# Kernel optimization log

Measured on AMD Instinct MI355X. Metric: run time of the kernel, lower is better.

Reference implementation:

```python
import jax, jax.numpy as jnp
import numpy as np

B, N, DIM = 2, 1024, 512
HEADS, DIM_HEAD = 8, 64
HIDDEN = HEADS * DIM_HEAD
TIME_DIM = 512
BIAS_DIM = 16
EPS = 1e-5


def setup_inputs() -> dict:
    key = jax.random.key(0)
    ks = jax.random.split(key, 12)
    inp = {
        "x": jax.random.normal(ks[0], (B, N, DIM), jnp.float32),
        "residx": jnp.broadcast_to(jnp.arange(N, dtype=jnp.float32), (B, N)),
        "time": jax.random.normal(ks[1], (B, 1, TIME_DIM), jnp.float32),
        "attn_bias": jax.random.normal(ks[2], (B, BIAS_DIM, N, N), jnp.float32),
        "seq_mask": jnp.ones((B, N), jnp.float32),
        # params
        "gamma": jnp.ones((DIM,), jnp.float32),
        "Wt": jax.random.normal(ks[3], (2 * DIM, TIME_DIM), jnp.float32) * 0.02,
        "bt": jax.random.normal(ks[4], (2 * DIM,), jnp.float32) * 0.02,
        "Wb": jax.random.normal(ks[5], (HEADS, BIAS_DIM), jnp.float32) * 0.1,
        "bb": jax.random.normal(ks[6], (HEADS,), jnp.float32) * 0.1,
        "Wq": jax.random.normal(ks[7], (HIDDEN, DIM), jnp.float32) * (DIM ** -0.5),
        "Wkv": jax.random.normal(ks[8], (2 * HIDDEN, DIM), jnp.float32) * (DIM ** -0.5),
        "Wo": jax.random.normal(ks[9], (DIM, HIDDEN), jnp.float32) * (HIDDEN ** -0.5),
    }
    return inp


def _layer_norm(x, gamma):
    mu = jnp.mean(x, axis=-1, keepdims=True)
    var = jnp.var(x, axis=-1, keepdims=True)
    return (x - mu) * jax.lax.rsqrt(var + EPS) * gamma  # beta buffer is zeros


def reference(x, residx, time, attn_bias, seq_mask, gamma, Wt, bt, Wb, bb, Wq, Wkv, Wo):
    h, d = HEADS, DIM_HEAD
    b, n, _ = x.shape
    xn = _layer_norm(x, gamma)
    # time conditioning: SiLU -> Linear -> chunk into scale/shift
    t = jax.nn.silu(time) @ Wt.T + bt  # [B,1,2*dim]
    scale, shift = jnp.split(t, 2, axis=-1)
    xn = xn * (scale + 1.0) + shift
    xn = xn * seq_mask[..., None]
    # projections
    q = (xn @ Wq.T).reshape(b, n, h, d).transpose(0, 2, 1, 3)  # b h n d
    kv = xn @ Wkv.T
    k_, v_ = jnp.split(kv, 2, axis=-1)
    k = k_.reshape(b, n, h, d).transpose(0, 2, 1, 3)
    v = v_.reshape(b, n, h, d).transpose(0, 2, 1, 3)
    q = q * (d ** -0.5)
    sim = jnp.einsum('bhid,bhjd->bhij', q, k)
    # attn bias projection: b a i j -> linear over a -> b h i j
    bias = jnp.einsum('baij,ha->bhij', attn_bias, Wb) + bb[None, :, None, None]
    sim = sim + bias
    # mask
    attn_mask = seq_mask[:, None, :, None] * seq_mask[:, None, None, :]  # b 1 i j
    sim = sim - (1.0 - attn_mask) * 1e6
    attn = jax.nn.softmax(sim, axis=-1)
    out = jnp.einsum('bhij,bhjd->bhid', attn, v)
    out = out.transpose(0, 2, 1, 3).reshape(b, n, h * d)
    out = out @ Wo.T
    out = out * seq_mask[..., None]
    return out
```

## Files before the change

### kernel.cpp

```cpp
#include <hip/hip_runtime.h>
#include <cstdint>
#include <cstddef>

typedef __bf16 bf16x8 __attribute__((ext_vector_type(8)));
typedef float f32x4 __attribute__((ext_vector_type(4)));
typedef unsigned short u16;
typedef unsigned short u16x8 __attribute__((ext_vector_type(8)));

__device__ __forceinline__ u16 f2b(float f) {
    union { float f; uint32_t u; } v; v.f = f;
    uint32_t r = v.u + 0x7fffu + ((v.u >> 16) & 1u);
    return (u16)(r >> 16);
}
__device__ __forceinline__ float b2f(u16 h) {
    union { uint32_t u; float f; } v; v.u = ((uint32_t)h) << 16; return v.f;
}

__global__ __launch_bounds__(256) void prep_kernel(
    const float* __restrict__ Wq, const float* __restrict__ Wkv, const float* __restrict__ Wo,
    const float* __restrict__ timep, const float* __restrict__ Wt, const float* __restrict__ bt,
    u16* __restrict__ wqkv, u16* __restrict__ wo, float* __restrict__ tbuf)
{
    __shared__ float st[512];
    int bx = blockIdx.x, tid = threadIdx.x;
    if (bx < 1024) {
        int i = bx * 256 + tid;
        float4 v; u16* dp;
        if (i < 65536)      { v = ((const float4*)Wq)[i];            dp = wqkv + (size_t)i * 4; }
        else if (i < 196608){ int k = i - 65536;  v = ((const float4*)Wkv)[k]; dp = wqkv + 262144 + (size_t)k * 4; }
        else                { int k = i - 196608; v = ((const float4*)Wo)[k];  dp = wo + (size_t)k * 4; }
        ushort4 o;
        o.x = f2b(v.x); o.y = f2b(v.y); o.z = f2b(v.z); o.w = f2b(v.w);
        *(ushort4*)dp = o;
    } else {
        int bx2 = bx - 1024;
        int b = bx2 >> 2, ch = bx2 & 3;
        for (int k = tid; k < 512; k += 256) {
            float v = timep[b * 512 + k];
            st[k] = v / (1.f + __expf(-v));
        }
        __syncthreads();
        int o = ch * 256 + tid;
        const float4* wrow = (const float4*)(Wt + (size_t)o * 512);
        float acc = bt[o];
        #pragma unroll 4
        for (int k4 = 0; k4 < 128; k4++) {
            float4 w = wrow[k4];
            acc += st[k4*4+0]*w.x + st[k4*4+1]*w.y + st[k4*4+2]*w.z + st[k4*4+3]*w.w;
        }
        tbuf[b * 1024 + o] = acc;
    }
}

__global__ __launch_bounds__(64) void ln_cond_kernel(
    const float* __restrict__ x, const float* __restrict__ gamma,
    const float* __restrict__ tbuf, const float* __restrict__ seq_mask,
    u16* __restrict__ xn)
{
    int m = blockIdx.x;
    int b = m >> 10;
    int lane = threadIdx.x;
    const float* xr = x + (size_t)m * 512;
    int c0 = lane * 8;
    float4 v0 = *(const float4*)(xr + c0);
    float4 v1 = *(const float4*)(xr + c0 + 4);
    float xv[8] = {v0.x, v0.y, v0.z, v0.w, v1.x, v1.y, v1.z, v1.w};
    float s = 0.f, ss = 0.f;
    #pragma unroll
    for (int e = 0; e < 8; e++) { s += xv[e]; ss += xv[e]*xv[e]; }
    #pragma unroll
    for (int off = 1; off < 64; off <<= 1) {
        s  += __shfl_xor(s, off);
        ss += __shfl_xor(ss, off);
    }
    float mu = s * (1.f/512.f);
    float var = ss * (1.f/512.f) - mu*mu;
    float rs = rsqrtf(var + 1e-5f);
    float mk = seq_mask[m];
    u16x8 ov;
    #pragma unroll
    for (int e = 0; e < 8; e++) {
        int c = c0 + e;
        float sc = tbuf[b*1024 + c] + 1.f;
        float sh = tbuf[b*1024 + 512 + c];
        float val = ((xv[e] - mu) * rs * gamma[c] * sc + sh) * mk;
        ov[e] = f2b(val);
    }
    *(u16x8*)&xn[(size_t)m * 512 + c0] = ov;
}

__global__ __launch_bounds__(256) void qkv_gemm_kernel(
    const u16* __restrict__ xn, const u16* __restrict__ wqkv,
    u16* __restrict__ qb, u16* __restrict__ kb, u16* __restrict__ vT)
{
    __shared__ u16 As[128][40];
    __shared__ u16 Bs[128][40];
    const int tid = threadIdx.x;
    const int lane = tid & 63, wid = tid >> 6;
    const int wr = wid >> 1, wc = wid & 1;
    const int li = lane & 15, g = lane >> 4;
    const int m0 = blockIdx.x * 128, n0 = blockIdx.y * 128;

    f32x4 acc[4][4] = {};
    const int srow = tid >> 2, scol = (tid & 3) * 8;
    for (int k0 = 0; k0 < 512; k0 += 32) {
        *(bf16x8*)&As[srow][scol]      = *(const bf16x8*)&xn[(size_t)(m0+srow)*512 + k0 + scol];
        *(bf16x8*)&As[srow+64][scol]   = *(const bf16x8*)&xn[(size_t)(m0+srow+64)*512 + k0 + scol];
        *(bf16x8*)&Bs[srow][scol]      = *(const bf16x8*)&wqkv[(size_t)(n0+srow)*512 + k0 + scol];
        *(bf16x8*)&Bs[srow+64][scol]   = *(const bf16x8*)&wqkv[(size_t)(n0+srow+64)*512 + k0 + scol];
        __syncthreads();
        bf16x8 a[4], bf[4];
        #pragma unroll
        for (int mi = 0; mi < 4; mi++) a[mi]  = *(const bf16x8*)&As[wr*64 + mi*16 + li][g*8];
        #pragma unroll
        for (int nj = 0; nj < 4; nj++) bf[nj] = *(const bf16x8*)&Bs[wc*64 + nj*16 + li][g*8];
        #pragma unroll
        for (int mi = 0; mi < 4; mi++)
            #pragma unroll
            for (int nj = 0; nj < 4; nj++)
                acc[mi][nj] = __builtin_amdgcn_mfma_f32_16x16x32_bf16(a[mi], bf[nj], acc[mi][nj], 0, 0, 0);
        __syncthreads();
    }
    #pragma unroll
    for (int mi = 0; mi < 4; mi++)
        #pragma unroll
        for (int nj = 0; nj < 4; nj++) {
            int o = n0 + wc*64 + nj*16 + li;
            int m_base = m0 + wr*64 + mi*16 + g*4;
            if (o < 1024) {
                #pragma unroll
                for (int r = 0; r < 4; r++) {
                    int m = m_base + r;
                    int b = m >> 10, n = m & 1023;
                    float v = acc[mi][nj][r];
                    if (o < 512) {
                        qb[((size_t)(b*8 + (o>>6))*1024 + n)*64 + (o&63)] = f2b(v * 0.125f);
                    } else {
                        int oo = o - 512;
                        kb[((size_t)(b*8 + (oo>>6))*1024 + n)*64 + (oo&63)] = f2b(v);
                    }
                }
            } else {
                int oo = o - 1024;
                int b = m_base >> 10, n = m_base & 1023;
                ushort4 ov;
                ov.x = f2b(acc[mi][nj][0]); ov.y = f2b(acc[mi][nj][1]);
                ov.z = f2b(acc[mi][nj][2]); ov.w = f2b(acc[mi][nj][3]);
                *(ushort4*)&vT[((size_t)(b*8 + (oo>>6))*64 + (oo&63))*1024 + n] = ov;
            }
        }
}

__global__ __launch_bounds__(256) void bias_kernel(
    const float* __restrict__ ab, const float* __restrict__ Wb,
    const float* __restrict__ bbv, u16* __restrict__ bias_t)
{
    __shared__ float wbs[128];
    __shared__ float bbs[8];
    int tid = threadIdx.x;
    if (tid < 128) wbs[tid] = Wb[tid];
    if (tid < 8) bbs[tid] = bbv[tid];
    __syncthreads();
    int t = blockIdx.x * 256 + tid;
    int b = t >> 16;
    int rem = t & 65535;
    int iq = rem >> 8, jq = rem & 255;
    int i = iq * 4, j = jq * 4;
    f32x4 acc[8][4];
    #pragma unroll
    for (int h = 0; h < 8; h++)
        #pragma unroll
        for (int r = 0; r < 4; r++) {
            float bv = bbs[h];
            acc[h][r][0] = bv; acc[h][r][1] = bv; acc[h][r][2] = bv; acc[h][r][3] = bv;
        }
    for (int a = 0; a < 16; a++) {
        f32x4 v[4];
        #pragma unroll
        for (int r = 0; r < 4; r++) {
            const f32x4* src = (const f32x4*)&ab[(((size_t)(b*16 + a)) << 20) + ((size_t)(i + r) << 10) + j];
            v[r] = __builtin_nontemporal_load(src);
        }
        #pragma unroll
        for (int h = 0; h < 8; h++) {
            float w = wbs[h*16 + a];
            #pragma unroll
            for (int r = 0; r < 4; r++) acc[h][r] += w * v[r];
        }
    }
    int it32 = iq >> 3, jt = jq >> 4;
    int isub = (iq >> 2) & 1, g = iq & 3;
    int li0 = (jq & 3) * 4, fj = (jq >> 2) & 3;
    #pragma unroll
    for (int h = 0; h < 8; h++) {
        size_t base = ((((size_t)(b*8 + h))*32 + it32)*16 + jt)*2048 + fj*4;
        #pragma unroll
        for (int c = 0; c < 4; c++) {
            ushort4 o;
            o.x = f2b(acc[h][0][c]); o.y = f2b(acc[h][1][c]);
            o.z = f2b(acc[h][2][c]); o.w = f2b(acc[h][3][c]);
            *(ushort4*)&bias_t[base + (size_t)(isub*64 + g*16 + li0 + c)*16] = o;
        }
    }
}

__global__ __launch_bounds__(256) void attn_kernel(
    const u16* __restrict__ qb, const u16* __restrict__ kb, const u16* __restrict__ vT,
    const u16* __restrict__ bias_t, const float* __restrict__ seq_mask,
    float* __restrict__ Om, float* __restrict__ ml)
{
    __shared__ u16 Qs[64][72];
    __shared__ u16 Ks[2][64][72];
    __shared__ u16 Vs[2][64][72];
    __shared__ u16 Ps[4][16][72];
    __shared__ float mjs[512];
    int tid = threadIdx.x;
    int lane = tid & 63, w = tid >> 6;
    int li = lane & 15, g = lane >> 4;
    int it = blockIdx.x, h = blockIdx.y;
    int bz = blockIdx.z;
    int b = bz >> 1, jh = bz & 1;
    int bh = b*8 + h;
    int i0 = it * 64;
    int jt0 = jh * 8;
    const u16* qp = qb + ((size_t)bh*1024 + i0) * 64;
    const u16* kp = kb + (size_t)bh*65536 + (size_t)jt0*4096;
    const u16* vp = vT + (size_t)bh*65536;
    const u16* bp = bias_t + (((size_t)(bh*32 + it*2 + (w>>1)))*16 + jt0)*2048 + ((w&1)*64 + lane)*16;

    *(bf16x8*)&Qs[tid>>2][(tid&3)*16]     = *(const bf16x8*)&qp[tid*16];
    *(bf16x8*)&Qs[tid>>2][(tid&3)*16 + 8] = *(const bf16x8*)&qp[tid*16 + 8];
    if (tid < 128) ((float4*)mjs)[tid] = ((const float4*)(seq_mask + b*1024 + jh*512))[tid];

    const int krow = tid >> 2, kcol = (tid & 3) * 16;
    const int vrow = tid >> 3, vcol = (tid & 7) * 8;

    bf16x8 kr0, kr1, vr0, vr1, bfA_c, bfB_c, bfA_n, bfB_n;
    #define LOADT(jx) do { \
        kr0 = *(const bf16x8*)&kp[(size_t)(jx)*4096 + tid*16]; \
        kr1 = *(const bf16x8*)&kp[(size_t)(jx)*4096 + tid*16 + 8]; \
        vr0 = *(const bf16x8*)&vp[(size_t)vrow*1024 + (jt0+(jx))*64 + vcol]; \
        vr1 = *(const bf16x8*)&vp[(size_t)(vrow+32)*1024 + (jt0+(jx))*64 + vcol]; \
        bfA_n = *(const bf16x8*)&bp[(size_t)(jx)*2048]; \
        bfB_n = *(const bf16x8*)&bp[(size_t)(jx)*2048 + 8]; \
    } while (0)
    #define STORET(buf_) do { \
        *(bf16x8*)&Ks[buf_][krow][kcol]     = kr0; \
        *(bf16x8*)&Ks[buf_][krow][kcol + 8] = kr1; \
        *(bf16x8*)&Vs[buf_][vrow][vcol]      = vr0; \
        *(bf16x8*)&Vs[buf_][vrow + 32][vcol] = vr1; \
    } while (0)

    f32x4 oacc[4] = {};
    float m_run[4], l_run[4], mi[4];
    #pragma unroll
    for (int r = 0; r < 4; r++) {
        m_run[r] = -3e38f; l_run[r] = 0.f;
        mi[r] = seq_mask[b*1024 + i0 + w*16 + g*4 + r];
    }

    LOADT(0); STORET(0); bfA_c = bfA_n; bfB_c = bfB_n;
    __syncthreads();

    for (int jtt = 0; jtt < 8; jtt++) {
        int cur = jtt & 1;
        if (jtt < 7) LOADT(jtt + 1);
        f32x4 s[4] = {};
        bf16x8 aq0 = *(const bf16x8*)&Qs[w*16 + li][g*8];
        bf16x8 aq1 = *(const bf16x8*)&Qs[w*16 + li][32 + g*8];
        #pragma unroll
        for (int fj = 0; fj < 4; fj++) {
            bf16x8 bk0 = *(const bf16x8*)&Ks[cur][fj*16 + li][g*8];
            bf16x8 bk1 = *(const bf16x8*)&Ks[cur][fj*16 + li][32 + g*8];
            s[fj] = __builtin_amdgcn_mfma_f32_16x16x32_bf16(aq0, bk0, s[fj], 0, 0, 0);
            s[fj] = __builtin_amdgcn_mfma_f32_16x16x32_bf16(aq1, bk1, s[fj], 0, 0, 0);
        }
        float pmax[4] = {-3e38f, -3e38f, -3e38f, -3e38f};
        #pragma unroll
        for (int fj = 0; fj < 4; fj++) {
            float mj = mjs[jtt*64 + fj*16 + li];
            #pragma unroll
            for (int r = 0; r < 4; r++) {
                float bvl = (fj < 2) ? b2f(((u16x8)bfA_c)[(fj&1)*4 + r]) : b2f(((u16x8)bfB_c)[(fj&1)*4 + r]);
                float sv = s[fj][r] + bvl;
                sv -= (1.f - mi[r]*mj) * 1e6f;
                s[fj][r] = sv;
                pmax[r] = fmaxf(pmax[r], sv);
            }
        }
        #pragma unroll
        for (int r = 0; r < 4; r++)
            #pragma unroll
            for (int off = 1; off < 16; off <<= 1)
                pmax[r] = fmaxf(pmax[r], __shfl_xor(pmax[r], off));
        float alpha[4], psum[4] = {0.f, 0.f, 0.f, 0.f}, mnew[4];
        #pragma unroll
        for (int r = 0; r < 4; r++) {
            mnew[r] = fmaxf(m_run[r], pmax[r]);
            alpha[r] = __expf(m_run[r] - mnew[r]);
            m_run[r] = mnew[r];
        }
        #pragma unroll
        for (int fj = 0; fj < 4; fj++)
            #pragma unroll
            for (int r = 0; r < 4; r++) {
                float p = __expf(s[fj][r] - mnew[r]);
                s[fj][r] = p;
                psum[r] += p;
            }
        #pragma unroll
        for (int r = 0; r < 4; r++) {
            #pragma unroll
            for (int off = 1; off < 16; off <<= 1) psum[r] += __shfl_xor(psum[r], off);
            l_run[r] = l_run[r]*alpha[r] + psum[r];
        }
        #pragma unroll
        for (int fj = 0; fj < 4; fj++)
            #pragma unroll
            for (int r = 0; r < 4; r++)
                Ps[w][g*4 + r][fj*16 + li] = f2b(s[fj][r]);
        #pragma unroll
        for (int fd = 0; fd < 4; fd++)
            #pragma unroll
            for (int r = 0; r < 4; r++)
                oacc[fd][r] *= alpha[r];
        bf16x8 ap0 = *(const bf16x8*)&Ps[w][li][g*8];
        bf16x8 ap1 = *(const bf16x8*)&Ps[w][li][32 + g*8];
        #pragma unroll
        for (int fd = 0; fd < 4; fd++) {
            bf16x8 bv0 = *(const bf16x8*)&Vs[cur][fd*16 + li][g*8];
            bf16x8 bv1 = *(const bf16x8*)&Vs[cur][fd*16 + li][32 + g*8];
            oacc[fd] = __builtin_amdgcn_mfma_f32_16x16x32_bf16(ap0, bv0, oacc[fd], 0, 0, 0);
            oacc[fd] = __builtin_amdgcn_mfma_f32_16x16x32_bf16(ap1, bv1, oacc[fd], 0, 0, 0);
        }
        if (jtt < 7) { STORET(cur ^ 1); bfA_c = bfA_n; bfB_c = bfB_n; }
        __syncthreads();
    }
    size_t pbase = ((size_t)(bh*16 + it)*2 + jh) * 4096;
    #pragma unroll
    for (int fd = 0; fd < 4; fd++)
        #pragma unroll
        for (int r = 0; r < 4; r++)
            Om[pbase + (size_t)(w*16 + g*4 + r)*64 + fd*16 + li] = oacc[fd][r];
    if (li == 0) {
        #pragma unroll
        for (int r = 0; r < 4; r++) {
            size_t mb = ((size_t)(bh*16 + it)*2 + jh) * 128 + (w*16 + g*4 + r)*2;
            ml[mb] = m_run[r]; ml[mb + 1] = l_run[r];
        }
    }
    #undef LOADT
    #undef STORET
}

__global__ __launch_bounds__(256) void merge_kernel(
    const float* __restrict__ Om, const float* __restrict__ ml, u16* __restrict__ aout)
{
    int blk = blockIdx.x;
    int bh = blk >> 4, it = blk & 15;
    int b = bh >> 3, h = bh & 7;
    int tid = threadIdx.x;
    int row = tid >> 2, dc = (tid & 3) * 16;
    size_t p0 = ((size_t)blk*2 + 0)*4096 + (size_t)row*64 + dc;
    size_t p1 = ((size_t)blk*2 + 1)*4096 + (size_t)row*64 + dc;
    size_t m0i = ((size_t)blk*2 + 0)*128 + row*2;
    size_t m1i = ((size_t)blk*2 + 1)*128 + row*2;
    float m0 = ml[m0i], l0 = ml[m0i + 1];
    float m1 = ml[m1i], l1 = ml[m1i + 1];
    float mm = fmaxf(m0, m1);
    float e0 = __expf(m0 - mm), e1 = __expf(m1 - mm);
    float linv = 1.f / (l0*e0 + l1*e1);
    int i = it*64 + row;
    u16* op = &aout[((size_t)(b*1024 + i))*512 + h*64 + dc];
    #pragma unroll
    for (int c4 = 0; c4 < 4; c4++) {
        f32x4 v0 = *(const f32x4*)&Om[p0 + c4*4];
        f32x4 v1 = *(const f32x4*)&Om[p1 + c4*4];
        ushort4 o;
        o.x = f2b((v0[0]*e0 + v1[0]*e1)*linv);
        o.y = f2b((v0[1]*e0 + v1[1]*e1)*linv);
        o.z = f2b((v0[2]*e0 + v1[2]*e1)*linv);
        o.w = f2b((v0[3]*e0 + v1[3]*e1)*linv);
        *(ushort4*)&op[c4*4] = o;
    }
}

__global__ __launch_bounds__(256) void out_gemm_kernel(
    const u16* __restrict__ aout, const u16* __restrict__ wo,
    const float* __restrict__ seq_mask, float* __restrict__ out)
{
    __shared__ u16 As[64][40];
    __shared__ u16 Bs[64][40];
    const int tid = threadIdx.x;
    const int lane = tid & 63, wid = tid >> 6;
    const int wr = wid >> 1, wc = wid & 1;
    const int li = lane & 15, g = lane >> 4;
    const int m0 = blockIdx.x * 64, n0 = blockIdx.y * 64;

    f32x4 acc[2][2] = {};
    const int lrow = tid >> 2, lcol = (tid & 3) * 8;
    for (int k0 = 0; k0 < 512; k0 += 32) {
        *(bf16x8*)&As[lrow][lcol] = *(const bf16x8*)&aout[(size_t)(m0+lrow)*512 + k0 + lcol];
        *(bf16x8*)&Bs[lrow][lcol] = *(const bf16x8*)&wo[(size_t)(n0+lrow)*512 + k0 + lcol];
        __syncthreads();
        bf16x8 a[2], bf[2];
        #pragma unroll
        for (int fi = 0; fi < 2; fi++) a[fi]  = *(const bf16x8*)&As[wr*32 + fi*16 + li][g*8];
        #pragma unroll
        for (int fj = 0; fj < 2; fj++) bf[fj] = *(const bf16x8*)&Bs[wc*32 + fj*16 + li][g*8];
        #pragma unroll
        for (int fi = 0; fi < 2; fi++)
            #pragma unroll
            for (int fj = 0; fj < 2; fj++)
                acc[fi][fj] = __builtin_amdgcn_mfma_f32_16x16x32_bf16(a[fi], bf[fj], acc[fi][fj], 0, 0, 0);
        __syncthreads();
    }
    #pragma unroll
    for (int fi = 0; fi < 2; fi++)
        #pragma unroll
        for (int fj = 0; fj < 2; fj++)
            #pragma unroll
            for (int r = 0; r < 4; r++) {
                int m = m0 + wr*32 + fi*16 + g*4 + r;
                int o = n0 + wc*32 + fj*16 + li;
                out[(size_t)m*512 + o] = acc[fi][fj][r] * seq_mask[m];
            }
}

extern "C" void kernel_launch(void* const* d_in, const int* in_sizes, int n_in,
                              void* d_out, int out_size, void* d_ws, size_t ws_size,
                              hipStream_t stream) {
    const float* x         = (const float*)d_in[0];
    const float* timep     = (const float*)d_in[2];
    const float* attn_bias = (const float*)d_in[3];
    const float* seq_mask  = (const float*)d_in[4];
    const float* gamma     = (const float*)d_in[5];
    const float* Wt        = (const float*)d_in[6];
    const float* bt        = (const float*)d_in[7];
    const float* Wb        = (const float*)d_in[8];
    const float* bb        = (const float*)d_in[9];
    const float* Wq        = (const float*)d_in[10];
    const float* Wkv       = (const float*)d_in[11];
    const float* Wo        = (const float*)d_in[12];
    float* out = (float*)d_out;

    char* ws = (char*)d_ws;
    size_t off = 0;
    auto alloc = [&](size_t bytes) { char* p = ws + off; off += (bytes + 255) & ~(size_t)255; return p; };
    float* tbuf  = (float*)alloc(2 * 1024 * 4);
    u16* xn      = (u16*)alloc((size_t)2048 * 512 * 2);
    u16* wqkv    = (u16*)alloc((size_t)1536 * 512 * 2);
    u16* wo      = (u16*)alloc((size_t)512 * 512 * 2);
    u16* qb      = (u16*)alloc((size_t)2 * 8 * 1024 * 64 * 2);
    u16* kb      = (u16*)alloc((size_t)2 * 8 * 1024 * 64 * 2);
    u16* vT      = (u16*)alloc((size_t)2 * 8 * 64 * 1024 * 2);
    u16* bias_t  = (u16*)alloc((size_t)2 * 8 * 1024 * 1024 * 2);
    u16* aout    = (u16*)alloc((size_t)2048 * 512 * 2);
    float* Om    = (float*)alloc((size_t)256 * 2 * 4096 * 4);
    float* ml    = (float*)alloc((size_t)256 * 2 * 128 * 4);
    (void)ws_size;

    prep_kernel<<<1032, 256, 0, stream>>>(Wq, Wkv, Wo, timep, Wt, bt, wqkv, wo, tbuf);
    ln_cond_kernel<<<2048, 64, 0, stream>>>(x, gamma, tbuf, seq_mask, xn);
    qkv_gemm_kernel<<<dim3(16, 12), 256, 0, stream>>>(xn, wqkv, qb, kb, vT);
    bias_kernel<<<512, 256, 0, stream>>>(attn_bias, Wb, bb, bias_t);
    attn_kernel<<<dim3(16, 8, 4), 256, 0, stream>>>(qb, kb, vT, bias_t, seq_mask, Om, ml);
    merge_kernel<<<256, 256, 0, stream>>>(Om, ml, aout);
    out_gemm_kernel<<<dim3(32, 8), 256, 0, stream>>>(aout, wo, seq_mask, out);
}
```

Baseline: 105.9 us.

## Merge QKV GEMM and bias projection into one launch; reswizzle attention LDS layout

Combines the bias-projection kernel and the QKV GEMM into a single launch that dispatches on block index, so the memory-bound bias work and the compute-bound GEMM can run concurrently and one launch gap disappears. In the attention kernel, Q fragments are now loaded straight into registers instead of staged through LDS. K, V and P tiles are stored in an MFMA-fragment-ordered flat layout to avoid LDS bank conflicts without padding. The cost is a larger kernel with divergent roles and higher register pressure in the fused kernel.

```diff
diff --git a/kernel.cpp b/kernel.cpp
--- a/kernel.cpp
+++ b/kernel.cpp
@@ -89,118 +89,116 @@
     *(u16x8*)&xn[(size_t)m * 512 + c0] = ov;
 }
 
-__global__ __launch_bounds__(256) void qkv_gemm_kernel(
+__global__ __launch_bounds__(256) void qkv_bias_kernel(
+    const float* __restrict__ ab, const float* __restrict__ Wb, const float* __restrict__ bbv,
     const u16* __restrict__ xn, const u16* __restrict__ wqkv,
-    u16* __restrict__ qb, u16* __restrict__ kb, u16* __restrict__ vT)
+    u16* __restrict__ bias_t, u16* __restrict__ qb, u16* __restrict__ kb, u16* __restrict__ vT)
 {
     __shared__ u16 As[128][40];
     __shared__ u16 Bs[128][40];
-    const int tid = threadIdx.x;
-    const int lane = tid & 63, wid = tid >> 6;
-    const int wr = wid >> 1, wc = wid & 1;
-    const int li = lane & 15, g = lane >> 4;
-    const int m0 = blockIdx.x * 128, n0 = blockIdx.y * 128;
-
-    f32x4 acc[4][4] = {};
-    const int srow = tid >> 2, scol = (tid & 3) * 8;
-    for (int k0 = 0; k0 < 512; k0 += 32) {
-        *(bf16x8*)&As[srow][scol]      = *(const bf16x8*)&xn[(size_t)(m0+srow)*512 + k0 + scol];
-        *(bf16x8*)&As[srow+64][scol]   = *(const bf16x8*)&xn[(size_t)(m0+srow+64)*512 + k0 + scol];
-        *(bf16x8*)&Bs[srow][scol]      = *(const bf16x8*)&wqkv[(size_t)(n0+srow)*512 + k0 + scol];
-        *(bf16x8*)&Bs[srow+64][scol]   = *(const bf16x8*)&wqkv[(size_t)(n0+srow+64)*512 + k0 + scol];
-        __syncthreads();
-        bf16x8 a[4], bf[4];
-        #pragma unroll
-        for (int mi = 0; mi < 4; mi++) a[mi]  = *(const bf16x8*)&As[wr*64 + mi*16 + li][g*8];
-        #pragma unroll
-        for (int nj = 0; nj < 4; nj++) bf[nj] = *(const bf16x8*)&Bs[wc*64 + nj*16 + li][g*8];
-        #pragma unroll
-        for (int mi = 0; mi < 4; mi++)
-            #pragma unroll
-            for (int nj = 0; nj < 4; nj++)
-                acc[mi][nj] = __builtin_amdgcn_mfma_f32_16x16x32_bf16(a[mi], bf[nj], acc[mi][nj], 0, 0, 0);
-        __syncthreads();
-    }
-    #pragma unroll
-    for (int mi = 0; mi < 4; mi++)
-        #pragma unroll
-        for (int nj = 0; nj < 4; nj++) {
-            int o = n0 + wc*64 + nj*16 + li;
-            int m_base = m0 + wr*64 + mi*16 + g*4;
-            if (o < 1024) {
-                #pragma unroll
-                for (int r = 0; r < 4; r++) {
-                    int m = m_base + r;
-                    int b = m >> 10, n = m & 1023;
-                    float v = acc[mi][nj][r];
-                    if (o < 512) {
-                        qb[((size_t)(b*8 + (o>>6))*1024 + n)*64 + (o&63)] = f2b(v * 0.125f);
-                    } else {
-                        int oo = o - 512;
-                        kb[((size_t)(b*8 + (oo>>6))*1024 + n)*64 + (oo&63)] = f2b(v);
-                    }
-                }
-            } else {
-                int oo = o - 1024;
-                int b = m_base >> 10, n = m_base & 1023;
-                ushort4 ov;
-                ov.x = f2b(acc[mi][nj][0]); ov.y = f2b(acc[mi][nj][1]);
-                ov.z = f2b(acc[mi][nj][2]); ov.w = f2b(acc[mi][nj][3]);
-                *(ushort4*)&vT[((size_t)(b*8 + (oo>>6))*64 + (oo&63))*1024 + n] = ov;
-            }
-        }
-}
-
-__global__ __launch_bounds__(256) void bias_kernel(
-    const float* __restrict__ ab, const float* __restrict__ Wb,
-    const float* __restrict__ bbv, u16* __restrict__ bias_t)
-{
     __shared__ float wbs[128];
     __shared__ float bbs[8];
-    int tid = threadIdx.x;
-    if (tid < 128) wbs[tid] = Wb[tid];
-    if (tid < 8) bbs[tid] = bbv[tid];
-    __syncthreads();
-    int t = blockIdx.x * 256 + tid;
-    int b = t >> 16;
-    int rem = t & 65535;
-    int iq = rem >> 8, jq = rem & 255;
-    int i = iq * 4, j = jq * 4;
-    f32x4 acc[8][4];
-    #pragma unroll
-    for (int h = 0; h < 8; h++)
-        #pragma unroll
-        for (int r = 0; r < 4; r++) {
-            float bv = bbs[h];
-            acc[h][r][0] = bv; acc[h][r][1] = bv; acc[h][r][2] = bv; acc[h][r][3] = bv;
-        }
-    for (int a = 0; a < 16; a++) {
-        f32x4 v[4];
-        #pragma unroll
-        for (int r = 0; r < 4; r++) {
-            const f32x4* src = (const f32x4*)&ab[(((size_t)(b*16 + a)) << 20) + ((size_t)(i + r) << 10) + j];
-            v[r] = __builtin_nontemporal_load(src);
-        }
+    const int tid = threadIdx.x;
+    const int bx = blockIdx.x;
+    if (bx < 512) {
+        if (tid < 128) wbs[tid] = Wb[tid];
+        if (tid < 8) bbs[tid] = bbv[tid];
+        __syncthreads();
+        int t = bx * 256 + tid;
+        int b = t >> 16;
+        int rem = t & 65535;
+        int iq = rem >> 8, jq = rem & 255;
+        int i = iq * 4, j = jq * 4;
+        f32x4 acc[8][4];
+        #pragma unroll
+        for (int h = 0; h < 8; h++)
+            #pragma unroll
+            for (int r = 0; r < 4; r++) {
+                float bv = bbs[h];
+                acc[h][r][0] = bv; acc[h][r][1] = bv; acc[h][r][2] = bv; acc[h][r][3] = bv;
+            }
+        for (int a = 0; a < 16; a++) {
+            f32x4 v[4];
+            #pragma unroll
+            for (int r = 0; r < 4; r++) {
+                const f32x4* src = (const f32x4*)&ab[(((size_t)(b*16 + a)) << 20) + ((size_t)(i + r) << 10) + j];
+                v[r] = __builtin_nontemporal_load(src);
+            }
+            #pragma unroll
+            for (int h = 0; h < 8; h++) {
+                float w = wbs[h*16 + a];
+                #pragma unroll
+                for (int r = 0; r < 4; r++) acc[h][r] += w * v[r];
+            }
+        }
+        int it32 = iq >> 3, jt = jq >> 4;
+        int isub = (iq >> 2) & 1, g = iq & 3;
+        int li0 = (jq & 3) * 4, fj = (jq >> 2) & 3;
         #pragma unroll
         for (int h = 0; h < 8; h++) {
-            float w = wbs[h*16 + a];
-            #pragma unroll
-            for (int r = 0; r < 4; r++) acc[h][r] += w * v[r];
-        }
-    }
-    int it32 = iq >> 3, jt = jq >> 4;
-    int isub = (iq >> 2) & 1, g = iq & 3;
-    int li0 = (jq & 3) * 4, fj = (jq >> 2) & 3;
-    #pragma unroll
-    for (int h = 0; h < 8; h++) {
-        size_t base = ((((size_t)(b*8 + h))*32 + it32)*16 + jt)*2048 + fj*4;
-        #pragma unroll
-        for (int c = 0; c < 4; c++) {
-            ushort4 o;
-            o.x = f2b(acc[h][0][c]); o.y = f2b(acc[h][1][c]);
-            o.z = f2b(acc[h][2][c]); o.w = f2b(acc[h][3][c]);
-            *(ushort4*)&bias_t[base + (size_t)(isub*64 + g*16 + li0 + c)*16] = o;
-        }
+            size_t base = ((((size_t)(b*8 + h))*32 + it32)*16 + jt)*2048 + fj*4;
+            #pragma unroll
+            for (int c = 0; c < 4; c++) {
+                ushort4 o;
+                o.x = f2b(acc[h][0][c]); o.y = f2b(acc[h][1][c]);
+                o.z = f2b(acc[h][2][c]); o.w = f2b(acc[h][3][c]);
+                *(ushort4*)&bias_t[base + (size_t)(isub*64 + g*16 + li0 + c)*16] = o;
+            }
+        }
+    } else {
+        int v = bx - 512;
+        const int m0 = (v & 15) * 128, n0 = (v >> 4) * 128;
+        const int lane = tid & 63, wid = tid >> 6;
+        const int wr = wid >> 1, wc = wid & 1;
+        const int li = lane & 15, g = lane >> 4;
+        f32x4 acc[4][4] = {};
+        const int srow = tid >> 2, scol = (tid & 3) * 8;
+        for (int k0 = 0; k0 < 512; k0 += 32) {
+            *(bf16x8*)&As[srow][scol]      = *(const bf16x8*)&xn[(size_t)(m0+srow)*512 + k0 + scol];
+            *(bf16x8*)&As[srow+64][scol]   = *(const bf16x8*)&xn[(size_t)(m0+srow+64)*512 + k0 + scol];
+            *(bf16x8*)&Bs[srow][scol]      = *(const bf16x8*)&wqkv[(size_t)(n0+srow)*512 + k0 + scol];
+            *(bf16x8*)&Bs[srow+64][scol]   = *(const bf16x8*)&wqkv[(size_t)(n0+srow+64)*512 + k0 + scol];
+            __syncthreads();
+            bf16x8 a[4], bf[4];
+            #pragma unroll
+            for (int mi = 0; mi < 4; mi++) a[mi]  = *(const bf16x8*)&As[wr*64 + mi*16 + li][g*8];
+            #pragma unroll
+            for (int nj = 0; nj < 4; nj++) bf[nj] = *(const bf16x8*)&Bs[wc*64 + nj*16 + li][g*8];
+            #pragma unroll
+            for (int mi = 0; mi < 4; mi++)
+                #pragma unroll
+                for (int nj = 0; nj < 4; nj++)
+                    acc[mi][nj] = __builtin_amdgcn_mfma_f32_16x16x32_bf16(a[mi], bf[nj], acc[mi][nj], 0, 0, 0);
+            __syncthreads();
+        }
+        #pragma unroll
+        for (int mi = 0; mi < 4; mi++)
+            #pragma unroll
+            for (int nj = 0; nj < 4; nj++) {
+                int o = n0 + wc*64 + nj*16 + li;
+                int m_base = m0 + wr*64 + mi*16 + g*4;
+                if (o < 1024) {
+                    #pragma unroll
+                    for (int r = 0; r < 4; r++) {
+                        int m = m_base + r;
+                        int b = m >> 10, n = m & 1023;
+                        float vv = acc[mi][nj][r];
+                        if (o < 512) {
+                            qb[((size_t)(b*8 + (o>>6))*1024 + n)*64 + (o&63)] = f2b(vv * 0.125f);
+                        } else {
+                            int oo = o - 512;
+                            kb[((size_t)(b*8 + (oo>>6))*1024 + n)*64 + (oo&63)] = f2b(vv);
+                        }
+                    }
+                } else {
+                    int oo = o - 1024;
+                    int b = m_base >> 10, n = m_base & 1023;
+                    ushort4 ov;
+                    ov.x = f2b(acc[mi][nj][0]); ov.y = f2b(acc[mi][nj][1]);
+                    ov.z = f2b(acc[mi][nj][2]); ov.w = f2b(acc[mi][nj][3]);
+                    *(ushort4*)&vT[((size_t)(b*8 + (oo>>6))*64 + (oo&63))*1024 + n] = ov;
+                }
+            }
     }
 }
 
@@ -209,10 +207,9 @@
     const u16* __restrict__ bias_t, const float* __restrict__ seq_mask,
     float* __restrict__ Om, float* __restrict__ ml)
 {
-    __shared__ u16 Qs[64][72];
-    __shared__ u16 Ks[2][64][72];
-    __shared__ u16 Vs[2][64][72];
-    __shared__ u16 Ps[4][16][72];
+    __shared__ u16 Ks[2][4096];
+    __shared__ u16 Vs[2][4096];
+    __shared__ u16 Ps[4][1024];
     __shared__ float mjs[512];
     int tid = threadIdx.x;
     int lane = tid & 63, w = tid >> 6;
@@ -228,27 +225,27 @@
     const u16* vp = vT + (size_t)bh*65536;
     const u16* bp = bias_t + (((size_t)(bh*32 + it*2 + (w>>1)))*16 + jt0)*2048 + ((w&1)*64 + lane)*16;
 
-    *(bf16x8*)&Qs[tid>>2][(tid&3)*16]     = *(const bf16x8*)&qp[tid*16];
-    *(bf16x8*)&Qs[tid>>2][(tid&3)*16 + 8] = *(const bf16x8*)&qp[tid*16 + 8];
     if (tid < 128) ((float4*)mjs)[tid] = ((const float4*)(seq_mask + b*1024 + jh*512))[tid];
 
-    const int krow = tid >> 2, kcol = (tid & 3) * 16;
-    const int vrow = tid >> 3, vcol = (tid & 7) * 8;
-
+    bf16x8 aq0 = *(const bf16x8*)&qp[(w*16 + li)*64 + g*8];
+    bf16x8 aq1 = *(const bf16x8*)&qp[(w*16 + li)*64 + 32 + g*8];
+
+    const int sli = tid & 15, sg = (tid >> 4) & 3, sf = tid >> 6;
+    const int kslot0 = (sf*128 + sg*16 + sli) * 8;
     bf16x8 kr0, kr1, vr0, vr1, bfA_c, bfB_c, bfA_n, bfB_n;
     #define LOADT(jx) do { \
-        kr0 = *(const bf16x8*)&kp[(size_t)(jx)*4096 + tid*16]; \
-        kr1 = *(const bf16x8*)&kp[(size_t)(jx)*4096 + tid*16 + 8]; \
-        vr0 = *(const bf16x8*)&vp[(size_t)vrow*1024 + (jt0+(jx))*64 + vcol]; \
-        vr1 = *(const bf16x8*)&vp[(size_t)(vrow+32)*1024 + (jt0+(jx))*64 + vcol]; \
+        kr0 = *(const bf16x8*)&kp[(size_t)(jx)*4096 + (sf*16 + sli)*64 + sg*8]; \
+        kr1 = *(const bf16x8*)&kp[(size_t)(jx)*4096 + (sf*16 + sli)*64 + 32 + sg*8]; \
+        vr0 = *(const bf16x8*)&vp[(size_t)(sf*16 + sli)*1024 + (jt0+(jx))*64 + sg*8]; \
+        vr1 = *(const bf16x8*)&vp[(size_t)(sf*16 + sli)*1024 + (jt0+(jx))*64 + 32 + sg*8]; \
         bfA_n = *(const bf16x8*)&bp[(size_t)(jx)*2048]; \
         bfB_n = *(const bf16x8*)&bp[(size_t)(jx)*2048 + 8]; \
     } while (0)
     #define STORET(buf_) do { \
-        *(bf16x8*)&Ks[buf_][krow][kcol]     = kr0; \
-        *(bf16x8*)&Ks[buf_][krow][kcol + 8] = kr1; \
-        *(bf16x8*)&Vs[buf_][vrow][vcol]      = vr0; \
-        *(bf16x8*)&Vs[buf_][vrow + 32][vcol] = vr1; \
+        *(bf16x8*)&Ks[buf_][kslot0]       = kr0; \
+        *(bf16x8*)&Ks[buf_][kslot0 + 512] = kr1; \
+        *(bf16x8*)&Vs[buf_][kslot0]       = vr0; \
+        *(bf16x8*)&Vs[buf_][kslot0 + 512] = vr1; \
     } while (0)
 
     f32x4 oacc[4] = {};
@@ -266,12 +263,10 @@
         int cur = jtt & 1;
         if (jtt < 7) LOADT(jtt + 1);
         f32x4 s[4] = {};
-        bf16x8 aq0 = *(const bf16x8*)&Qs[w*16 + li][g*8];
-        bf16x8 aq1 = *(const bf16x8*)&Qs[w*16 + li][32 + g*8];
         #pragma unroll
         for (int fj = 0; fj < 4; fj++) {
-            bf16x8 bk0 = *(const bf16x8*)&Ks[cur][fj*16 + li][g*8];
-            bf16x8 bk1 = *(const bf16x8*)&Ks[cur][fj*16 + li][32 + g*8];
+            bf16x8 bk0 = *(const bf16x8*)&Ks[cur][(fj*128 + g*16 + li)*8];
+            bf16x8 bk1 = *(const bf16x8*)&Ks[cur][(fj*128 + g*16 + li)*8 + 512];
             s[fj] = __builtin_amdgcn_mfma_f32_16x16x32_bf16(aq0, bk0, s[fj], 0, 0, 0);
             s[fj] = __builtin_amdgcn_mfma_f32_16x16x32_bf16(aq1, bk1, s[fj], 0, 0, 0);
         }
@@ -315,21 +310,25 @@
             l_run[r] = l_run[r]*alpha[r] + psum[r];
         }
         #pragma unroll
-        for (int fj = 0; fj < 4; fj++)
+        for (int fj = 0; fj < 4; fj++) {
+            int ph2 = fj >> 1;
+            int pg = (fj*2 + (li >> 3)) & 3;
+            int pin = li & 7;
             #pragma unroll
             for (int r = 0; r < 4; r++)
-                Ps[w][g*4 + r][fj*16 + li] = f2b(s[fj][r]);
+                Ps[w][(ph2*64 + pg*16 + g*4 + r)*8 + pin] = f2b(s[fj][r]);
+        }
         #pragma unroll
         for (int fd = 0; fd < 4; fd++)
             #pragma unroll
             for (int r = 0; r < 4; r++)
                 oacc[fd][r] *= alpha[r];
-        bf16x8 ap0 = *(const bf16x8*)&Ps[w][li][g*8];
-        bf16x8 ap1 = *(const bf16x8*)&Ps[w][li][32 + g*8];
+        bf16x8 ap0 = *(const bf16x8*)&Ps[w][(g*16 + li)*8];
+        bf16x8 ap1 = *(const bf16x8*)&Ps[w][(g*16 + li)*8 + 512];
         #pragma unroll
         for (int fd = 0; fd < 4; fd++) {
-            bf16x8 bv0 = *(const bf16x8*)&Vs[cur][fd*16 + li][g*8];
-            bf16x8 bv1 = *(const bf16x8*)&Vs[cur][fd*16 + li][32 + g*8];
+            bf16x8 bv0 = *(const bf16x8*)&Vs[cur][(fd*128 + g*16 + li)*8];
+            bf16x8 bv1 = *(const bf16x8*)&Vs[cur][(fd*128 + g*16 + li)*8 + 512];
             oacc[fd] = __builtin_amdgcn_mfma_f32_16x16x32_bf16(ap0, bv0, oacc[fd], 0, 0, 0);
             oacc[fd] = __builtin_amdgcn_mfma_f32_16x16x32_bf16(ap1, bv1, oacc[fd], 0, 0, 0);
         }
@@ -462,8 +461,7 @@
 
     prep_kernel<<<1032, 256, 0, stream>>>(Wq, Wkv, Wo, timep, Wt, bt, wqkv, wo, tbuf);
     ln_cond_kernel<<<2048, 64, 0, stream>>>(x, gamma, tbuf, seq_mask, xn);
-    qkv_gemm_kernel<<<dim3(16, 12), 256, 0, stream>>>(xn, wqkv, qb, kb, vT);
-    bias_kernel<<<512, 256, 0, stream>>>(attn_bias, Wb, bb, bias_t);
+    qkv_bias_kernel<<<704, 256, 0, stream>>>(attn_bias, Wb, bb, xn, wqkv, bias_t, qb, kb, vT);
     attn_kernel<<<dim3(16, 8, 4), 256, 0, stream>>>(qb, kb, vT, bias_t, seq_mask, Om, ml);
     merge_kernel<<<256, 256, 0, stream>>>(Om, ml, aout);
     out_gemm_kernel<<<dim3(32, 8), 256, 0, stream>>>(aout, wo, seq_mask, out);
```

Result: faster. 101.4 us (-4.2%).
